# Kernel optimization log

Hardware: AMD Instinct MI355X
Metric: run time of the kernel (lower is better)

## Reference

```python
import jax, jax.numpy as jnp
import numpy as np

Q_SCALE = 64  # 1 << 6, from quantize_8bit default
Q_STEP = 2.0 / Q_SCALE
Q_MIN = -(2 ** 7) / Q_SCALE      # -128/64 = -2.0
Q_MAX = (2 ** 7 - 1) / Q_SCALE   # 127/64


def quantize_8bit(x):
    # round-to-step with straight-through estimator (matches slayer quantize), then clamp
    xq = x + jax.lax.stop_gradient(jnp.round(x / Q_STEP) * Q_STEP - x)
    return jnp.clip(xq, Q_MIN, Q_MAX)


def weight_norm(v, g):
    # per-output-channel weight norm: w = g * v / ||v||  (v: [out, in])
    n = jnp.sqrt(jnp.sum(v * v, axis=1, keepdims=True))
    return g[:, None] * v / n


def sigma_delta_block(x, v, g, clamp6):
    # x: [N, Cin, H, W, T]
    qw = quantize_8bit(weight_norm(v, g))           # [Cout, Cin], 8-bit quantized
    y = jnp.einsum('oi,nihwt->nohwt', qw, x)        # 1x1x1 conv (pointwise)
    s = jnp.cumsum(y, axis=-1)                      # sigma unit: accumulate over time
    mean = jnp.mean(s, axis=(0, 2, 3, 4), keepdims=True)  # mean-only batchnorm
    a = s - mean
    if clamp6:                                      # Clamp6 activation (fc2); Ind = identity (fc1)
        a = jnp.clip(a, -6.0, 6.0)
    # delta unit, threshold=0: d[t] = a[t] - a[t-1], a[-1] = 0
    d = jnp.diff(a, axis=-1, prepend=jnp.zeros_like(a[..., :1]))
    return d


def setup_inputs() -> dict:
    key = jax.random.key(0)
    k = jax.random.split(key, 5)
    N, C, H, W, T = 4, 128, 32, 32, 32
    Cs = 32
    x = jax.random.normal(k[0], (N, C, H, W, T), dtype=jnp.float32)
    v1 = jax.random.normal(k[1], (Cs, C), dtype=jnp.float32) * 0.1
    g1 = jax.random.uniform(k[2], (Cs,), dtype=jnp.float32) + 0.5
    v2 = jax.random.normal(k[3], (C, Cs), dtype=jnp.float32) * 0.1
    g2 = jax.random.uniform(k[4], (C,), dtype=jnp.float32) + 0.5
    return {'x': x, 'v1': v1, 'g1': g1, 'v2': v2, 'g2': g2}


def reference(x, v1, g1, v2, g2):
    h = sigma_delta_block(x, v1, g1, clamp6=False)   # fc1: Ind activation
    out = sigma_delta_block(h, v2, g2, clamp6=True)  # fc2: Clamp6 activation
    return out
```

## Files before the change

kernel.cpp:

```cpp
#include <hip/hip_runtime.h>
#include <hip/hip_cooperative_groups.h>

namespace cg = cooperative_groups;

#define CIN  128
#define CHUNKF 32768

typedef float f32x4 __attribute__((ext_vector_type(4)));
typedef short s16x8 __attribute__((ext_vector_type(8)));


__device__ __forceinline__ uint pack_hilo(float f) {
  uint b = __float_as_uint(f);
  uint hi = b & 0xffff0000u;
  float lo = f - __uint_as_float(hi);
  return (hi >> 16) | (__float_as_uint(lo) & 0xffff0000u);
}

__global__ __launch_bounds__(256) void wnorm_mean_kernel(
    const float* __restrict__ x,
    const float* __restrict__ v1, const float* __restrict__ g1,
    const float* __restrict__ v2, const float* __restrict__ g2,
    float* __restrict__ ws) {
  int tid = threadIdx.x;
  if (blockIdx.x < 2048) {
    int b = blockIdx.x;
    int chunk = b >> 2, quarter = b & 3;
    int i = chunk & 127;
    const float4* xp = (const float4*)(x + (size_t)chunk * CHUNKF + (size_t)quarter * 8192);
    float acc = 0.f;
#pragma unroll
    for (int it = 0; it < 8; ++it) {
      int f4i = tid + 256 * it;
      float4 v = xp[f4i];
      int t0 = (4 * f4i) & 31;
      acc += v.x * (float)(32 - t0) + v.y * (float)(31 - t0)
           + v.z * (float)(30 - t0) + v.w * (float)(29 - t0);
    }
    for (int off = 32; off >= 1; off >>= 1) acc += __shfl_down(acc, off);
    __shared__ float part[4];
    if ((tid & 63) == 0) part[tid >> 6] = acc;
    __syncthreads();
    if (tid == 0) atomicAdd(&ws[8192 + i], part[0] + part[1] + part[2] + part[3]);
  } else {
    int b = blockIdx.x - 2048;
    bool first = (b < 32);
    int row = first ? b : b - 32;
    int len = first ? 128 : 32;
    const float* v = first ? v1 : v2;
    const float* g = first ? g1 : g2;
    double val = 0.0;
    if (tid < len) { double t = (double)v[row * len + tid]; val = t * t; }
    for (int off = 32; off >= 1; off >>= 1) val += __shfl_down(val, off);
    __shared__ double partial[4];
    if ((tid & 63) == 0) partial[tid >> 6] = val;
    __syncthreads();
    double norm = sqrt(partial[0] + partial[1]);
    if (tid < len) {
      double w = (double)g[row] * (double)v[row * len + tid] / norm;
      double qd = rint(w * 32.0) * 0.03125;
      qd = fmin(fmax(qd, -2.0), 1.984375);
      float qf = (float)qd;
      ushort bf = (ushort)(__float_as_uint(qf) >> 16);
      if (first) {
        ws[row * 128 + tid] = qf;
        ((ushort*)(ws + 8448))[row * 128 + tid] = bf;
      } else {
        ws[4096 + row * 32 + tid] = qf;
        ((ushort*)(ws + 10496))[row * 32 + tid] = bf;
      }
    }
  }
}

__global__ __launch_bounds__(256, 4) void fused_kernel(
    const float* __restrict__ x, const float* __restrict__ ws,
    float* __restrict__ out) {
  const ushort* qw1bf = (const ushort*)(ws + 8448);
  const ushort* qw2bf = (const ushort*)(ws + 10496);

  __shared__ uint xs[8192];
  __shared__ float zred[288];
  __shared__ float kls[128];

  const int tid = threadIdx.x;
  const int wv = tid >> 6;
  const int l  = tid & 63;
  const int g  = l >> 4;
  const int ln = l & 15;

  const int nb  = blockIdx.x >> 8;
  const int hw0 = (blockIdx.x & 255) * 4;
  const float* xblk = x + (size_t)nb * CIN * CHUNKF + (size_t)hw0 * 32;

  float4 xr[8];
#pragma unroll
  for (int k = 0; k < 8; ++k) {
    int f = k * 256 + tid, c = f >> 5, n4 = f & 31;
    xr[k] = *(const float4*)(xblk + (size_t)c * CHUNKF + n4 * 4);
  }

  s16x8 A1[2][4];
#pragma unroll
  for (int jt = 0; jt < 2; ++jt)
#pragma unroll
    for (int ks = 0; ks < 4; ++ks)
      A1[jt][ks] = *(const s16x8*)(qw1bf + (jt * 16 + ln) * 128 + ks * 32 + g * 8);

  {
    int j = tid & 31, grp = tid >> 5;
    const float* qr = ws + j * 128 + grp * 16;
    const float* mr = ws + 8192 + grp * 16;
    float pp = 0.f;
#pragma unroll
    for (int cc = 0; cc < 16; ++cc) pp += qr[cc] * mr[cc];
    zred[j * 8 + grp] = pp;
  }
  __syncthreads();
  if (tid < 32) {
    float t = 0.f;
#pragma unroll
    for (int gg = 0; gg < 8; ++gg) t += zred[tid * 8 + gg];
    zred[256 + tid] = t * (1.0f / 131072.0f);
  }
  __syncthreads();
  if (tid < 128) {
    const float* q2 = ws + 4096 + tid * 32;
    float kk = 0.f;
#pragma unroll 8
    for (int j = 0; j < 32; ++j) kk += q2[j] * zred[256 + j];
    kls[tid] = kk;
  }

  f32x4 acc1[2][2];
#pragma unroll
  for (int a = 0; a < 2; ++a)
#pragma unroll
    for (int b = 0; b < 2; ++b) acc1[a][b] = (f32x4){0.f, 0.f, 0.f, 0.f};

#pragma unroll
  for (int ph = 0; ph < 2; ++ph) {
#pragma unroll
    for (int k = 0; k < 8; ++k) {
      int f = k * 256 + tid, c = f >> 5, n4 = f & 31;
      int u = n4 ^ ((c >> 2) & 6);
      uint4 pk;
      pk.x = pack_hilo(xr[k].x); pk.y = pack_hilo(xr[k].y);
      pk.z = pack_hilo(xr[k].z); pk.w = pack_hilo(xr[k].w);
      *(uint4*)&xs[c * 128 + u * 4] = pk;
    }
    __syncthreads();
    if (ph == 0) {
#pragma unroll
      for (int k = 0; k < 8; ++k) {
        int f = k * 256 + tid, c = f >> 5, n4 = f & 31;
        xr[k] = *(const float4*)(xblk + (size_t)(64 + c) * CHUNKF + n4 * 4);
      }
    }
#pragma unroll
    for (int kl = 0; kl < 2; ++kl) {
#pragma unroll
      for (int nt = 0; nt < 2; ++nt) {
        const int n = wv * 32 + nt * 16 + ln;
        const int base = (kl * 32 + g * 8) * 128;
        const int u = ((n >> 2) ^ (((kl * 32 + g * 8) >> 2) & 6)) * 4 + (n & 3);
        uint q0 = xs[base + 0 * 128 + u], q1 = xs[base + 1 * 128 + u];
        uint q2 = xs[base + 2 * 128 + u], q3 = xs[base + 3 * 128 + u];
        uint q4 = xs[base + 4 * 128 + u], q5 = xs[base + 5 * 128 + u];
        uint q6 = xs[base + 6 * 128 + u], q7 = xs[base + 7 * 128 + u];
        uint4 H, L;
        H.x = (q0 & 0xffffu) | (q1 << 16);  H.y = (q2 & 0xffffu) | (q3 << 16);
        H.z = (q4 & 0xffffu) | (q5 << 16);  H.w = (q6 & 0xffffu) | (q7 << 16);
        L.x = (q0 >> 16) | (q1 & 0xffff0000u); L.y = (q2 >> 16) | (q3 & 0xffff0000u);
        L.z = (q4 >> 16) | (q5 & 0xffff0000u); L.w = (q6 >> 16) | (q7 & 0xffff0000u);
        s16x8 Bh = __builtin_bit_cast(s16x8, H);
        s16x8 Bl = __builtin_bit_cast(s16x8, L);
#pragma unroll
        for (int jt = 0; jt < 2; ++jt) {
          acc1[jt][nt] = __builtin_amdgcn_mfma_f32_16x16x32_bf16(A1[jt][ph * 2 + kl], Bh, acc1[jt][nt], 0, 0, 0);
          acc1[jt][nt] = __builtin_amdgcn_mfma_f32_16x16x32_bf16(A1[jt][ph * 2 + kl], Bl, acc1[jt][nt], 0, 0, 0);
        }
      }
    }
    __syncthreads();
  }

  uint* zw = xs + wv * 1024;
#pragma unroll
  for (int jt = 0; jt < 2; ++jt)
#pragma unroll
    for (int nt = 0; nt < 2; ++nt) {
      int n = nt * 16 + ln;
      int u = (jt * 4 + g) ^ (n & 7);
      uint4 pk;
      pk.x = pack_hilo(acc1[jt][nt][0]);
      pk.y = pack_hilo(acc1[jt][nt][1]);
      pk.z = pack_hilo(acc1[jt][nt][2]);
      pk.w = pack_hilo(acc1[jt][nt][3]);
      *(uint4*)&zw[n * 32 + u * 4] = pk;
    }

  s16x8 Ah[2], Al[2];
#pragma unroll
  for (int mt = 0; mt < 2; ++mt) {
    int n = mt * 16 + ln;
    int u0 = (2 * g) ^ (n & 7);
    int u1 = (2 * g + 1) ^ (n & 7);
    uint4 qa = *(const uint4*)&zw[n * 32 + u0 * 4];
    uint4 qb = *(const uint4*)&zw[n * 32 + u1 * 4];
    uint4 H, L;
    H.x = (qa.x & 0xffffu) | (qa.y << 16);  H.y = (qa.z & 0xffffu) | (qa.w << 16);
    H.z = (qb.x & 0xffffu) | (qb.y << 16);  H.w = (qb.z & 0xffffu) | (qb.w << 16);
    L.x = (qa.x >> 16) | (qa.y & 0xffff0000u); L.y = (qa.z >> 16) | (qa.w & 0xffff0000u);
    L.z = (qb.x >> 16) | (qb.y & 0xffff0000u); L.w = (qb.z >> 16) | (qb.w & 0xffff0000u);
    Ah[mt] = __builtin_bit_cast(s16x8, H);
    Al[mt] = __builtin_bit_cast(s16x8, L);
  }

  const size_t outbase = (size_t)nb * CIN * CHUNKF + (size_t)(hw0 + wv) * 32;
#pragma unroll 1
  for (int h = 0; h < 2; ++h) {
    s16x8 B2[4];
#pragma unroll
    for (int q = 0; q < 4; ++q)
      B2[q] = *(const s16x8*)(qw2bf + ((h * 4 + q) * 16 + ln) * 32 + g * 8);
    f32x4 acc2[4][2];
#pragma unroll
    for (int a = 0; a < 4; ++a)
#pragma unroll
      for (int b = 0; b < 2; ++b) acc2[a][b] = (f32x4){0.f, 0.f, 0.f, 0.f};
#pragma unroll
    for (int mt = 0; mt < 2; ++mt)
#pragma unroll
      for (int q = 0; q < 4; ++q) {
        acc2[q][mt] = __builtin_amdgcn_mfma_f32_16x16x32_bf16(Ah[mt], B2[q], acc2[q][mt], 0, 0, 0);
        acc2[q][mt] = __builtin_amdgcn_mfma_f32_16x16x32_bf16(Al[mt], B2[q], acc2[q][mt], 0, 0, 0);
      }
#pragma unroll
    for (int q = 0; q < 4; ++q) {
      const int nt = h * 4 + q;
      float c0[2], c1[2], c2[2], c3[2], base[2], Qi0 = 0.f;
#pragma unroll
      for (int mt = 0; mt < 2; ++mt) {
        c0[mt] = acc2[q][mt][0];
        c1[mt] = c0[mt] + acc2[q][mt][1];
        c2[mt] = c1[mt] + acc2[q][mt][2];
        c3[mt] = c2[mt] + acc2[q][mt][3];
        float Qi = c3[mt];
        float t1 = __shfl_up(Qi, 16); if (g >= 1) Qi += t1;
        float t2 = __shfl_up(Qi, 32); if (g >= 2) Qi += t2;
        base[mt] = Qi - c3[mt];
        if (mt == 0) Qi0 = Qi;
      }
      float S0tot = __shfl(Qi0, 48 + ln);
      base[1] += S0tot;
      const float kpp = kls[nt * 16 + ln];
      float* op = out + outbase + (size_t)(nt * 16 + ln) * CHUNKF;
#pragma unroll
      for (int mt = 0; mt < 2; ++mt) {
        float Bv = base[mt] - kpp;
        float prev = fminf(fmaxf(Bv, -6.f), 6.f);
        if (mt == 0 && g == 0) prev = 0.f;
        float A0 = fminf(fmaxf(Bv + c0[mt], -6.f), 6.f);
        float A1v = fminf(fmaxf(Bv + c1[mt], -6.f), 6.f);
        float A2v = fminf(fmaxf(Bv + c2[mt], -6.f), 6.f);
        float A3v = fminf(fmaxf(Bv + c3[mt], -6.f), 6.f);
        *(float4*)(op + mt * 16 + g * 4) =
            make_float4(A0 - prev, A1v - A0, A2v - A1v, A3v - A2v);
      }
    }
  }
}

__global__ __launch_bounds__(256, 2) void fused_all(
    const float* __restrict__ x,
    const float* __restrict__ v1, const float* __restrict__ g1,
    const float* __restrict__ v2, const float* __restrict__ g2,
    float* __restrict__ ws, float* __restrict__ out) {
  __shared__ uint xs[8192];
  __shared__ float mls[128];
  __shared__ float zred[256];
  __shared__ float zsm[32];
  __shared__ float kls[128];
  __shared__ double wpart[4];

  const int tid = threadIdx.x;
  const int bid = blockIdx.x;
  const int nb  = bid >> 7;
  const int hw8 = (bid & 127) * 8;
  float* msumP = ws + 8192;

  {
    const int l63 = tid & 63, wvp = tid >> 6;
    const int t0 = (4 * l63) & 31;
    const float wt0 = (float)(32 - t0), wt1 = (float)(31 - t0);
    const float wt2 = (float)(30 - t0), wt3 = (float)(29 - t0);
    const int slot = bid & 31;
    const float* xsl = x + (size_t)nb * CIN * CHUNKF + (size_t)hw8 * 32 + l63 * 4;
#pragma unroll 4
    for (int k = 0; k < 32; ++k) {
      int c = k * 4 + wvp;
      float4 v = *(const float4*)(xsl + (size_t)c * CHUNKF);
      float pv = v.x * wt0 + v.y * wt1 + v.z * wt2 + v.w * wt3;
      pv += __shfl_down(pv, 32);
      pv += __shfl_down(pv, 16);
      pv += __shfl_down(pv, 8);
      pv += __shfl_down(pv, 4);
      pv += __shfl_down(pv, 2);
      pv += __shfl_down(pv, 1);
      if (l63 == 0) atomicAdd(&msumP[slot * 128 + c], pv);
    }
  }

  if (bid < 160) {
    bool first = (bid < 32);
    int row = first ? bid : bid - 32;
    int len = first ? 128 : 32;
    const float* v = first ? v1 : v2;
    const float* g = first ? g1 : g2;
    double val = 0.0;
    if (tid < len) { double t = (double)v[row * len + tid]; val = t * t; }
    for (int off = 32; off >= 1; off >>= 1) val += __shfl_down(val, off);
    if ((tid & 63) == 0) wpart[tid >> 6] = val;
    __syncthreads();
    double norm = sqrt(wpart[0] + wpart[1]);
    if (tid < len) {
      double w = (double)g[row] * (double)v[row * len + tid] / norm;
      double qd = rint(w * 32.0) * 0.03125;
      qd = fmin(fmax(qd, -2.0), 1.984375);
      float qf = (float)qd;
      ushort bf = (ushort)(__float_as_uint(qf) >> 16);
      if (first) {
        ws[row * 128 + tid] = qf;
        ((ushort*)(ws + 12544))[row * 128 + tid] = bf;
      } else {
        ws[4096 + row * 32 + tid] = qf;
        ((ushort*)(ws + 14592))[row * 32 + tid] = bf;
      }
    }
  }

  cg::this_grid().sync();

  const ushort* qw1bf = (const ushort*)(ws + 12544);
  const ushort* qw2bf = (const ushort*)(ws + 14592);
  const int wv = tid >> 6;
  const int l  = tid & 63;
  const int g  = l >> 4;
  const int ln = l & 15;

  s16x8 A1[2][4];
#pragma unroll
  for (int jt = 0; jt < 2; ++jt)
#pragma unroll
    for (int ks = 0; ks < 4; ++ks)
      A1[jt][ks] = *(const s16x8*)(qw1bf + (jt * 16 + ln) * 128 + ks * 32 + g * 8);

  float4 xr[8];
  {
    const float* xg = x + (size_t)nb * CIN * CHUNKF + (size_t)hw8 * 32;
#pragma unroll
    for (int k = 0; k < 8; ++k) {
      int f = k * 256 + tid, c = f >> 5, n4 = f & 31;
      xr[k] = *(const float4*)(xg + (size_t)c * CHUNKF + n4 * 4);
    }
  }

  if (tid < 128) {
    float m = 0.f;
#pragma unroll
    for (int p = 0; p < 32; ++p) m += msumP[p * 128 + tid];
    mls[tid] = m;
  }
  __syncthreads();
  {
    int j = tid & 31, grp8 = tid >> 5;
    const float* qr = ws + j * 128 + grp8 * 16;
    float pp = 0.f;
#pragma unroll
    for (int cc = 0; cc < 16; ++cc) pp += qr[cc] * mls[grp8 * 16 + cc];
    zred[j * 8 + grp8] = pp;
  }
  __syncthreads();
  if (tid < 32) {
    float t = 0.f;
#pragma unroll
    for (int gg = 0; gg < 8; ++gg) t += zred[tid * 8 + gg];
    zsm[tid] = t * (1.0f / 131072.0f);
  }
  __syncthreads();
  if (tid < 128) {
    const float* q2p = ws + 4096 + tid * 32;
    float kk = 0.f;
#pragma unroll 8
    for (int j = 0; j < 32; ++j) kk += q2p[j] * zsm[j];
    kls[tid] = kk;
  }

#pragma unroll 1
  for (int grp = 0; grp < 2; ++grp) {
    const int hw0 = hw8 + grp * 4;
    const float* xg = x + (size_t)nb * CIN * CHUNKF + (size_t)hw0 * 32;

    f32x4 acc1[2][2];
#pragma unroll
    for (int a = 0; a < 2; ++a)
#pragma unroll
      for (int b = 0; b < 2; ++b) acc1[a][b] = (f32x4){0.f, 0.f, 0.f, 0.f};

    __syncthreads();

#pragma unroll
    for (int ph = 0; ph < 2; ++ph) {
#pragma unroll
      for (int k = 0; k < 8; ++k) {
        int f = k * 256 + tid, c = f >> 5, n4 = f & 31;
        int u = n4 ^ ((c >> 2) & 6);
        uint4 pk;
        pk.x = pack_hilo(xr[k].x); pk.y = pack_hilo(xr[k].y);
        pk.z = pack_hilo(xr[k].z); pk.w = pack_hilo(xr[k].w);
        *(uint4*)&xs[c * 128 + u * 4] = pk;
      }
      __syncthreads();
      if (ph == 0) {
#pragma unroll
        for (int k = 0; k < 8; ++k) {
          int f = k * 256 + tid, c = f >> 5, n4 = f & 31;
          xr[k] = *(const float4*)(xg + (size_t)(64 + c) * CHUNKF + n4 * 4);
        }
      }
#pragma unroll
      for (int kl = 0; kl < 2; ++kl) {
#pragma unroll
        for (int nt = 0; nt < 2; ++nt) {
          const int n = wv * 32 + nt * 16 + ln;
          const int base = (kl * 32 + g * 8) * 128;
          const int u = ((n >> 2) ^ (((kl * 32 + g * 8) >> 2) & 6)) * 4 + (n & 3);
          uint q0 = xs[base + 0 * 128 + u], q1 = xs[base + 1 * 128 + u];
          uint q2 = xs[base + 2 * 128 + u], q3 = xs[base + 3 * 128 + u];
          uint q4 = xs[base + 4 * 128 + u], q5 = xs[base + 5 * 128 + u];
          uint q6 = xs[base + 6 * 128 + u], q7 = xs[base + 7 * 128 + u];
          uint4 H, L;
          H.x = (q0 & 0xffffu) | (q1 << 16);  H.y = (q2 & 0xffffu) | (q3 << 16);
          H.z = (q4 & 0xffffu) | (q5 << 16);  H.w = (q6 & 0xffffu) | (q7 << 16);
          L.x = (q0 >> 16) | (q1 & 0xffff0000u); L.y = (q2 >> 16) | (q3 & 0xffff0000u);
          L.z = (q4 >> 16) | (q5 & 0xffff0000u); L.w = (q6 >> 16) | (q7 & 0xffff0000u);
          s16x8 Bh = __builtin_bit_cast(s16x8, H);
          s16x8 Bl = __builtin_bit_cast(s16x8, L);
#pragma unroll
          for (int jt = 0; jt < 2; ++jt) {
            acc1[jt][nt] = __builtin_amdgcn_mfma_f32_16x16x32_bf16(A1[jt][ph * 2 + kl], Bh, acc1[jt][nt], 0, 0, 0);
            acc1[jt][nt] = __builtin_amdgcn_mfma_f32_16x16x32_bf16(A1[jt][ph * 2 + kl], Bl, acc1[jt][nt], 0, 0, 0);
          }
        }
      }
      __syncthreads();
    }

    uint* zw = xs + wv * 1024;
#pragma unroll
    for (int jt = 0; jt < 2; ++jt)
#pragma unroll
      for (int nt = 0; nt < 2; ++nt) {
        int n = nt * 16 + ln;
        int u = (jt * 4 + g) ^ (n & 7);
        uint4 pk;
        pk.x = pack_hilo(acc1[jt][nt][0]);
        pk.y = pack_hilo(acc1[jt][nt][1]);
        pk.z = pack_hilo(acc1[jt][nt][2]);
        pk.w = pack_hilo(acc1[jt][nt][3]);
        *(uint4*)&zw[n * 32 + u * 4] = pk;
      }

    s16x8 Ah[2], Al[2];
#pragma unroll
    for (int mt = 0; mt < 2; ++mt) {
      int n = mt * 16 + ln;
      int u0 = (2 * g) ^ (n & 7);
      int u1 = (2 * g + 1) ^ (n & 7);
      uint4 qa = *(const uint4*)&zw[n * 32 + u0 * 4];
      uint4 qb = *(const uint4*)&zw[n * 32 + u1 * 4];
      uint4 H, L;
      H.x = (qa.x & 0xffffu) | (qa.y << 16);  H.y = (qa.z & 0xffffu) | (qa.w << 16);
      H.z = (qb.x & 0xffffu) | (qb.y << 16);  H.w = (qb.z & 0xffffu) | (qb.w << 16);
      L.x = (qa.x >> 16) | (qa.y & 0xffff0000u); L.y = (qa.z >> 16) | (qa.w & 0xffff0000u);
      L.z = (qb.x >> 16) | (qb.y & 0xffff0000u); L.w = (qb.z >> 16) | (qb.w & 0xffff0000u);
      Ah[mt] = __builtin_bit_cast(s16x8, H);
      Al[mt] = __builtin_bit_cast(s16x8, L);
    }

    if (grp == 0) {
      const float* xg1 = x + (size_t)nb * CIN * CHUNKF + (size_t)(hw8 + 4) * 32;
#pragma unroll
      for (int k = 0; k < 8; ++k) {
        int f = k * 256 + tid, c = f >> 5, n4 = f & 31;
        xr[k] = *(const float4*)(xg1 + (size_t)c * CHUNKF + n4 * 4);
      }
    }

    const size_t outbase = (size_t)nb * CIN * CHUNKF + (size_t)(hw0 + wv) * 32;
#pragma unroll 1
    for (int h = 0; h < 2; ++h) {
      s16x8 B2[4];
#pragma unroll
      for (int q = 0; q < 4; ++q)
        B2[q] = *(const s16x8*)(qw2bf + ((h * 4 + q) * 16 + ln) * 32 + g * 8);
      f32x4 acc2[4][2];
#pragma unroll
      for (int a = 0; a < 4; ++a)
#pragma unroll
        for (int b = 0; b < 2; ++b) acc2[a][b] = (f32x4){0.f, 0.f, 0.f, 0.f};
#pragma unroll
      for (int mt = 0; mt < 2; ++mt)
#pragma unroll
        for (int q = 0; q < 4; ++q) {
          acc2[q][mt] = __builtin_amdgcn_mfma_f32_16x16x32_bf16(Ah[mt], B2[q], acc2[q][mt], 0, 0, 0);
          acc2[q][mt] = __builtin_amdgcn_mfma_f32_16x16x32_bf16(Al[mt], B2[q], acc2[q][mt], 0, 0, 0);
        }
#pragma unroll
      for (int q = 0; q < 4; ++q) {
        const int nt = h * 4 + q;
        float c0[2], c1[2], c2[2], c3[2], base[2], Qi0 = 0.f;
#pragma unroll
        for (int mt = 0; mt < 2; ++mt) {
          c0[mt] = acc2[q][mt][0];
          c1[mt] = c0[mt] + acc2[q][mt][1];
          c2[mt] = c1[mt] + acc2[q][mt][2];
          c3[mt] = c2[mt] + acc2[q][mt][3];
          float Qi = c3[mt];
          float t1 = __shfl_up(Qi, 16); if (g >= 1) Qi += t1;
          float t2 = __shfl_up(Qi, 32); if (g >= 2) Qi += t2;
          base[mt] = Qi - c3[mt];
          if (mt == 0) Qi0 = Qi;
        }
        float S0tot = __shfl(Qi0, 48 + ln);
        base[1] += S0tot;
        const float kpp = kls[nt * 16 + ln];
        float* op = out + outbase + (size_t)(nt * 16 + ln) * CHUNKF;
#pragma unroll
        for (int mt = 0; mt < 2; ++mt) {
          float Bv = base[mt] - kpp;
          float prev = fminf(fmaxf(Bv, -6.f), 6.f);
          if (mt == 0 && g == 0) prev = 0.f;
          float A0 = fminf(fmaxf(Bv + c0[mt], -6.f), 6.f);
          float A1v = fminf(fmaxf(Bv + c1[mt], -6.f), 6.f);
          float A2v = fminf(fmaxf(Bv + c2[mt], -6.f), 6.f);
          float A3v = fminf(fmaxf(Bv + c3[mt], -6.f), 6.f);
          *(float4*)(op + mt * 16 + g * 4) =
              make_float4(A0 - prev, A1v - A0, A2v - A1v, A3v - A2v);
        }
      }
    }
  }
}

extern "C" void kernel_launch(void* const* d_in, const int* in_sizes, int n_in,
                              void* d_out, int out_size, void* d_ws, size_t ws_size,
                              hipStream_t stream) {
  const float* x  = (const float*)d_in[0];
  const float* v1 = (const float*)d_in[1];
  const float* g1 = (const float*)d_in[2];
  const float* v2 = (const float*)d_in[3];
  const float* g2 = (const float*)d_in[4];
  float* ws  = (float*)d_ws;
  float* out = (float*)d_out;

  hipMemsetAsync(ws + 8192, 0, 4096 * sizeof(float), stream);

  int dev = 0, coop = 0, occ = 0;
  hipGetDevice(&dev);
  hipDeviceGetAttribute(&coop, hipDeviceAttributeCooperativeLaunch, dev);
  hipOccupancyMaxActiveBlocksPerMultiprocessor(&occ, fused_all, 256, 0);

  if (coop && occ >= 2) {
    void* args[] = { (void*)&x, (void*)&v1, (void*)&g1, (void*)&v2, (void*)&g2,
                     (void*)&ws, (void*)&out };
    hipError_t e = hipLaunchCooperativeKernel((const void*)fused_all, dim3(512),
                                              dim3(256), args, 0, stream);
    if (e == hipSuccess) return;
  }

  wnorm_mean_kernel<<<2208, 256, 0, stream>>>(x, v1, g1, v2, g2, ws);
  fused_kernel<<<1024, 256, 0, stream>>>(x, ws, out);
}
```

Before: 49.28 us.

## Replace cooperative grid sync with atomic-counter spin barrier and split weight-norm kernel

Drops the cooperative launch and grid.sync in favour of a small weight-norm/init kernel plus a 1024-block main kernel. The main kernel increments a global counter after its mean-partial atomics, then spins on that counter before it needs the mean. Stage-1 MFMA work runs before the wait, so the global reduction overlaps with compute. Each block now handles 4 hw positions instead of 8, targeting 4 blocks per CU. The spin barrier relies on all 1024 blocks being co-resident, which is only guarded by an occupancy check, and it has a guard counter that can silently give wrong results on timeout. The fallback path now memsets only 128 floats instead of 4096, which may leave stale partial sums.

```diff
diff --git a/kernel.cpp b/kernel.cpp
--- a/kernel.cpp
+++ b/kernel.cpp
@@ -1,7 +1,4 @@
 #include <hip/hip_runtime.h>
-#include <hip/hip_cooperative_groups.h>
-
-namespace cg = cooperative_groups;
 
 #define CIN  128
 #define CHUNKF 32768
@@ -15,6 +12,283 @@
   uint hi = b & 0xffff0000u;
   float lo = f - __uint_as_float(hi);
   return (hi >> 16) | (__float_as_uint(lo) & 0xffff0000u);
+}
+
+__global__ __launch_bounds__(128) void wnorm_init(
+    const float* __restrict__ v1, const float* __restrict__ g1,
+    const float* __restrict__ v2, const float* __restrict__ g2,
+    float* __restrict__ ws) {
+  int b = blockIdx.x, tid = threadIdx.x;
+  if (b < 32) ws[8192 + b * 128 + tid] = 0.f;
+  if (b == 32 && tid == 0) *(uint*)(ws + 12288) = 0u;
+  bool first = (b < 32);
+  int row = first ? b : b - 32;
+  int len = first ? 128 : 32;
+  const float* v = first ? v1 : v2;
+  const float* g = first ? g1 : g2;
+
+  double val = 0.0;
+  if (tid < len) { double t = (double)v[row * len + tid]; val = t * t; }
+  for (int off = 32; off >= 1; off >>= 1) val += __shfl_down(val, off);
+  __shared__ double partial[2];
+  if ((tid & 63) == 0) partial[tid >> 6] = val;
+  __syncthreads();
+  double norm = sqrt(partial[0] + partial[1]);
+  if (tid < len) {
+    double w = (double)g[row] * (double)v[row * len + tid] / norm;
+    double qd = rint(w * 32.0) * 0.03125;
+    qd = fmin(fmax(qd, -2.0), 1.984375);
+    float qf = (float)qd;
+    ushort bf = (ushort)(__float_as_uint(qf) >> 16);
+    if (first) {
+      ws[row * 128 + tid] = qf;
+      ((ushort*)(ws + 12544))[row * 128 + tid] = bf;
+    } else {
+      ws[4096 + row * 32 + tid] = qf;
+      ((ushort*)(ws + 14592))[row * 32 + tid] = bf;
+    }
+  }
+}
+
+__global__ __launch_bounds__(256, 4) void fused_main(
+    const float* __restrict__ x, float* __restrict__ ws,
+    float* __restrict__ out) {
+  const ushort* qw1bf = (const ushort*)(ws + 12544);
+  const ushort* qw2bf = (const ushort*)(ws + 14592);
+
+  __shared__ uint xs[8192];
+  __shared__ float mls[128];
+  __shared__ float zred[288];
+  __shared__ float kls[128];
+
+  const int tid = threadIdx.x;
+  const int wv = tid >> 6;
+  const int l  = tid & 63;
+  const int g  = l >> 4;
+  const int ln = l & 15;
+
+  const int nb  = blockIdx.x >> 8;
+  const int hw0 = (blockIdx.x & 255) * 4;
+  const float* xblk = x + (size_t)nb * CIN * CHUNKF + (size_t)hw0 * 32;
+  float* msumP = ws + 8192;
+
+  {
+    const int l31 = tid & 31;
+    const int t0 = (l31 & 7) * 4;
+    const float wt0 = (float)(32 - t0), wt1 = (float)(31 - t0);
+    const float wt2 = (float)(30 - t0), wt3 = (float)(29 - t0);
+    const int slot = blockIdx.x & 31;
+#pragma unroll 4
+    for (int k = 0; k < 16; ++k) {
+      int c = k * 8 + (tid >> 5);
+      float4 v = *(const float4*)(xblk + (size_t)c * CHUNKF + l31 * 4);
+      float pv = v.x * wt0 + v.y * wt1 + v.z * wt2 + v.w * wt3;
+      pv += __shfl_down(pv, 16, 32);
+      pv += __shfl_down(pv, 8, 32);
+      pv += __shfl_down(pv, 4, 32);
+      pv += __shfl_down(pv, 2, 32);
+      pv += __shfl_down(pv, 1, 32);
+      if (l31 == 0) atomicAdd(&msumP[slot * 128 + c], pv);
+    }
+  }
+  __threadfence();
+  __syncthreads();
+  if (tid == 0) atomicAdd((uint*)(ws + 12288), 1u);
+
+  float4 xr[8];
+#pragma unroll
+  for (int k = 0; k < 8; ++k) {
+    int f = k * 256 + tid, c = f >> 5, n4 = f & 31;
+    xr[k] = *(const float4*)(xblk + (size_t)c * CHUNKF + n4 * 4);
+  }
+
+  s16x8 A1[2][4];
+#pragma unroll
+  for (int jt = 0; jt < 2; ++jt)
+#pragma unroll
+    for (int ks = 0; ks < 4; ++ks)
+      A1[jt][ks] = *(const s16x8*)(qw1bf + (jt * 16 + ln) * 128 + ks * 32 + g * 8);
+
+  f32x4 acc1[2][2];
+#pragma unroll
+  for (int a = 0; a < 2; ++a)
+#pragma unroll
+    for (int b = 0; b < 2; ++b) acc1[a][b] = (f32x4){0.f, 0.f, 0.f, 0.f};
+
+#pragma unroll
+  for (int ph = 0; ph < 2; ++ph) {
+#pragma unroll
+    for (int k = 0; k < 8; ++k) {
+      int f = k * 256 + tid, c = f >> 5, n4 = f & 31;
+      int u = n4 ^ ((c >> 2) & 6);
+      uint4 pk;
+      pk.x = pack_hilo(xr[k].x); pk.y = pack_hilo(xr[k].y);
+      pk.z = pack_hilo(xr[k].z); pk.w = pack_hilo(xr[k].w);
+      *(uint4*)&xs[c * 128 + u * 4] = pk;
+    }
+    __syncthreads();
+    if (ph == 0) {
+#pragma unroll
+      for (int k = 0; k < 8; ++k) {
+        int f = k * 256 + tid, c = f >> 5, n4 = f & 31;
+        xr[k] = *(const float4*)(xblk + (size_t)(64 + c) * CHUNKF + n4 * 4);
+      }
+    }
+#pragma unroll
+    for (int kl = 0; kl < 2; ++kl) {
+#pragma unroll
+      for (int nt = 0; nt < 2; ++nt) {
+        const int n = wv * 32 + nt * 16 + ln;
+        const int base = (kl * 32 + g * 8) * 128;
+        const int u = ((n >> 2) ^ (((kl * 32 + g * 8) >> 2) & 6)) * 4 + (n & 3);
+        uint q0 = xs[base + 0 * 128 + u], q1 = xs[base + 1 * 128 + u];
+        uint q2 = xs[base + 2 * 128 + u], q3 = xs[base + 3 * 128 + u];
+        uint q4 = xs[base + 4 * 128 + u], q5 = xs[base + 5 * 128 + u];
+        uint q6 = xs[base + 6 * 128 + u], q7 = xs[base + 7 * 128 + u];
+        uint4 H, L;
+        H.x = (q0 & 0xffffu) | (q1 << 16);  H.y = (q2 & 0xffffu) | (q3 << 16);
+        H.z = (q4 & 0xffffu) | (q5 << 16);  H.w = (q6 & 0xffffu) | (q7 << 16);
+        L.x = (q0 >> 16) | (q1 & 0xffff0000u); L.y = (q2 >> 16) | (q3 & 0xffff0000u);
+        L.z = (q4 >> 16) | (q5 & 0xffff0000u); L.w = (q6 >> 16) | (q7 & 0xffff0000u);
+        s16x8 Bh = __builtin_bit_cast(s16x8, H);
+        s16x8 Bl = __builtin_bit_cast(s16x8, L);
+#pragma unroll
+        for (int jt = 0; jt < 2; ++jt) {
+          acc1[jt][nt] = __builtin_amdgcn_mfma_f32_16x16x32_bf16(A1[jt][ph * 2 + kl], Bh, acc1[jt][nt], 0, 0, 0);
+          acc1[jt][nt] = __builtin_amdgcn_mfma_f32_16x16x32_bf16(A1[jt][ph * 2 + kl], Bl, acc1[jt][nt], 0, 0, 0);
+        }
+      }
+    }
+    __syncthreads();
+  }
+
+  uint* zw = xs + wv * 1024;
+#pragma unroll
+  for (int jt = 0; jt < 2; ++jt)
+#pragma unroll
+    for (int nt = 0; nt < 2; ++nt) {
+      int n = nt * 16 + ln;
+      int u = (jt * 4 + g) ^ (n & 7);
+      uint4 pk;
+      pk.x = pack_hilo(acc1[jt][nt][0]);
+      pk.y = pack_hilo(acc1[jt][nt][1]);
+      pk.z = pack_hilo(acc1[jt][nt][2]);
+      pk.w = pack_hilo(acc1[jt][nt][3]);
+      *(uint4*)&zw[n * 32 + u * 4] = pk;
+    }
+
+  s16x8 Ah[2], Al[2];
+#pragma unroll
+  for (int mt = 0; mt < 2; ++mt) {
+    int n = mt * 16 + ln;
+    int u0 = (2 * g) ^ (n & 7);
+    int u1 = (2 * g + 1) ^ (n & 7);
+    uint4 qa = *(const uint4*)&zw[n * 32 + u0 * 4];
+    uint4 qb = *(const uint4*)&zw[n * 32 + u1 * 4];
+    uint4 H, L;
+    H.x = (qa.x & 0xffffu) | (qa.y << 16);  H.y = (qa.z & 0xffffu) | (qa.w << 16);
+    H.z = (qb.x & 0xffffu) | (qb.y << 16);  H.w = (qb.z & 0xffffu) | (qb.w << 16);
+    L.x = (qa.x >> 16) | (qa.y & 0xffff0000u); L.y = (qa.z >> 16) | (qa.w & 0xffff0000u);
+    L.z = (qb.x >> 16) | (qb.y & 0xffff0000u); L.w = (qb.z >> 16) | (qb.w & 0xffff0000u);
+    Ah[mt] = __builtin_bit_cast(s16x8, H);
+    Al[mt] = __builtin_bit_cast(s16x8, L);
+  }
+
+  if (tid == 0) {
+    const uint* dc = (const uint*)(ws + 12288);
+    int guard = 0;
+    while (__hip_atomic_load(dc, __ATOMIC_ACQUIRE, __HIP_MEMORY_SCOPE_AGENT) < 1024u
+           && ++guard < 10000000) { }
+  }
+  __syncthreads();
+  __threadfence();
+  if (tid < 128) {
+    float m = 0.f;
+#pragma unroll
+    for (int p = 0; p < 32; ++p)
+      m += __hip_atomic_load(&msumP[p * 128 + tid], __ATOMIC_RELAXED,
+                             __HIP_MEMORY_SCOPE_AGENT);
+    mls[tid] = m * (1.0f / 131072.0f);
+  }
+  __syncthreads();
+  {
+    int j = tid & 31, grp = tid >> 5;
+    const float* qr = ws + j * 128 + grp * 16;
+    float pp = 0.f;
+#pragma unroll
+    for (int cc = 0; cc < 16; ++cc) pp += qr[cc] * mls[grp * 16 + cc];
+    zred[j * 8 + grp] = pp;
+  }
+  __syncthreads();
+  if (tid < 32) {
+    float t = 0.f;
+#pragma unroll
+    for (int gg = 0; gg < 8; ++gg) t += zred[tid * 8 + gg];
+    zred[256 + tid] = t;
+  }
+  __syncthreads();
+  if (tid < 128) {
+    const float* q2 = ws + 4096 + tid * 32;
+    float kk = 0.f;
+#pragma unroll 8
+    for (int j = 0; j < 32; ++j) kk += q2[j] * zred[256 + j];
+    kls[tid] = kk;
+  }
+  __syncthreads();
+
+  const size_t outbase = (size_t)nb * CIN * CHUNKF + (size_t)(hw0 + wv) * 32;
+#pragma unroll 1
+  for (int h = 0; h < 2; ++h) {
+    s16x8 B2[4];
+#pragma unroll
+    for (int q = 0; q < 4; ++q)
+      B2[q] = *(const s16x8*)(qw2bf + ((h * 4 + q) * 16 + ln) * 32 + g * 8);
+    f32x4 acc2[4][2];
+#pragma unroll
+    for (int a = 0; a < 4; ++a)
+#pragma unroll
+      for (int b = 0; b < 2; ++b) acc2[a][b] = (f32x4){0.f, 0.f, 0.f, 0.f};
+#pragma unroll
+    for (int mt = 0; mt < 2; ++mt)
+#pragma unroll
+      for (int q = 0; q < 4; ++q) {
+        acc2[q][mt] = __builtin_amdgcn_mfma_f32_16x16x32_bf16(Ah[mt], B2[q], acc2[q][mt], 0, 0, 0);
+        acc2[q][mt] = __builtin_amdgcn_mfma_f32_16x16x32_bf16(Al[mt], B2[q], acc2[q][mt], 0, 0, 0);
+      }
+#pragma unroll
+    for (int q = 0; q < 4; ++q) {
+      const int nt = h * 4 + q;
+      float c0[2], c1[2], c2[2], c3[2], base[2], Qi0 = 0.f;
+#pragma unroll
+      for (int mt = 0; mt < 2; ++mt) {
+        c0[mt] = acc2[q][mt][0];
+        c1[mt] = c0[mt] + acc2[q][mt][1];
+        c2[mt] = c1[mt] + acc2[q][mt][2];
+        c3[mt] = c2[mt] + acc2[q][mt][3];
+        float Qi = c3[mt];
+        float t1 = __shfl_up(Qi, 16); if (g >= 1) Qi += t1;
+        float t2 = __shfl_up(Qi, 32); if (g >= 2) Qi += t2;
+        base[mt] = Qi - c3[mt];
+        if (mt == 0) Qi0 = Qi;
+      }
+      float S0tot = __shfl(Qi0, 48 + ln);
+      base[1] += S0tot;
+      const float kpp = kls[nt * 16 + ln];
+      float* op = out + outbase + (size_t)(nt * 16 + ln) * CHUNKF;
+#pragma unroll
+      for (int mt = 0; mt < 2; ++mt) {
+        float Bv = base[mt] - kpp;
+        float prev = fminf(fmaxf(Bv, -6.f), 6.f);
+        if (mt == 0 && g == 0) prev = 0.f;
+        float A0 = fminf(fmaxf(Bv + c0[mt], -6.f), 6.f);
+        float A1v = fminf(fmaxf(Bv + c1[mt], -6.f), 6.f);
+        float A2v = fminf(fmaxf(Bv + c2[mt], -6.f), 6.f);
+        float A3v = fminf(fmaxf(Bv + c3[mt], -6.f), 6.f);
+        *(float4*)(op + mt * 16 + g * 4) =
+            make_float4(A0 - prev, A1v - A0, A2v - A1v, A3v - A2v);
+      }
+    }
+  }
 }
 
 __global__ __launch_bounds__(256) void wnorm_mean_kernel(
@@ -272,288 +546,6 @@
   }
 }
 
-__global__ __launch_bounds__(256, 2) void fused_all(
-    const float* __restrict__ x,
-    const float* __restrict__ v1, const float* __restrict__ g1,
-    const float* __restrict__ v2, const float* __restrict__ g2,
-    float* __restrict__ ws, float* __restrict__ out) {
-  __shared__ uint xs[8192];
-  __shared__ float mls[128];
-  __shared__ float zred[256];
-  __shared__ float zsm[32];
-  __shared__ float kls[128];
-  __shared__ double wpart[4];
-
-  const int tid = threadIdx.x;
-  const int bid = blockIdx.x;
-  const int nb  = bid >> 7;
-  const int hw8 = (bid & 127) * 8;
-  float* msumP = ws + 8192;
-
-  {
-    const int l63 = tid & 63, wvp = tid >> 6;
-    const int t0 = (4 * l63) & 31;
-    const float wt0 = (float)(32 - t0), wt1 = (float)(31 - t0);
-    const float wt2 = (float)(30 - t0), wt3 = (float)(29 - t0);
-    const int slot = bid & 31;
-    const float* xsl = x + (size_t)nb * CIN * CHUNKF + (size_t)hw8 * 32 + l63 * 4;
-#pragma unroll 4
-    for (int k = 0; k < 32; ++k) {
-      int c = k * 4 + wvp;
-      float4 v = *(const float4*)(xsl + (size_t)c * CHUNKF);
-      float pv = v.x * wt0 + v.y * wt1 + v.z * wt2 + v.w * wt3;
-      pv += __shfl_down(pv, 32);
-      pv += __shfl_down(pv, 16);
-      pv += __shfl_down(pv, 8);
-      pv += __shfl_down(pv, 4);
-      pv += __shfl_down(pv, 2);
-      pv += __shfl_down(pv, 1);
-      if (l63 == 0) atomicAdd(&msumP[slot * 128 + c], pv);
-    }
-  }
-
-  if (bid < 160) {
-    bool first = (bid < 32);
-    int row = first ? bid : bid - 32;
-    int len = first ? 128 : 32;
-    const float* v = first ? v1 : v2;
-    const float* g = first ? g1 : g2;
-    double val = 0.0;
-    if (tid < len) { double t = (double)v[row * len + tid]; val = t * t; }
-    for (int off = 32; off >= 1; off >>= 1) val += __shfl_down(val, off);
-    if ((tid & 63) == 0) wpart[tid >> 6] = val;
-    __syncthreads();
-    double norm = sqrt(wpart[0] + wpart[1]);
-    if (tid < len) {
-      double w = (double)g[row] * (double)v[row * len + tid] / norm;
-      double qd = rint(w * 32.0) * 0.03125;
-      qd = fmin(fmax(qd, -2.0), 1.984375);
-      float qf = (float)qd;
-      ushort bf = (ushort)(__float_as_uint(qf) >> 16);
-      if (first) {
-        ws[row * 128 + tid] = qf;
-        ((ushort*)(ws + 12544))[row * 128 + tid] = bf;
-      } else {
-        ws[4096 + row * 32 + tid] = qf;
-        ((ushort*)(ws + 14592))[row * 32 + tid] = bf;
-      }
-    }
-  }
-
-  cg::this_grid().sync();
-
-  const ushort* qw1bf = (const ushort*)(ws + 12544);
-  const ushort* qw2bf = (const ushort*)(ws + 14592);
-  const int wv = tid >> 6;
-  const int l  = tid & 63;
-  const int g  = l >> 4;
-  const int ln = l & 15;
-
-  s16x8 A1[2][4];
-#pragma unroll
-  for (int jt = 0; jt < 2; ++jt)
-#pragma unroll
-    for (int ks = 0; ks < 4; ++ks)
-      A1[jt][ks] = *(const s16x8*)(qw1bf + (jt * 16 + ln) * 128 + ks * 32 + g * 8);
-
-  float4 xr[8];
-  {
-    const float* xg = x + (size_t)nb * CIN * CHUNKF + (size_t)hw8 * 32;
-#pragma unroll
-    for (int k = 0; k < 8; ++k) {
-      int f = k * 256 + tid, c = f >> 5, n4 = f & 31;
-      xr[k] = *(const float4*)(xg + (size_t)c * CHUNKF + n4 * 4);
-    }
-  }
-
-  if (tid < 128) {
-    float m = 0.f;
-#pragma unroll
-    for (int p = 0; p < 32; ++p) m += msumP[p * 128 + tid];
-    mls[tid] = m;
-  }
-  __syncthreads();
-  {
-    int j = tid & 31, grp8 = tid >> 5;
-    const float* qr = ws + j * 128 + grp8 * 16;
-    float pp = 0.f;
-#pragma unroll
-    for (int cc = 0; cc < 16; ++cc) pp += qr[cc] * mls[grp8 * 16 + cc];
-    zred[j * 8 + grp8] = pp;
-  }
-  __syncthreads();
-  if (tid < 32) {
-    float t = 0.f;
-#pragma unroll
-    for (int gg = 0; gg < 8; ++gg) t += zred[tid * 8 + gg];
-    zsm[tid] = t * (1.0f / 131072.0f);
-  }
-  __syncthreads();
-  if (tid < 128) {
-    const float* q2p = ws + 4096 + tid * 32;
-    float kk = 0.f;
-#pragma unroll 8
-    for (int j = 0; j < 32; ++j) kk += q2p[j] * zsm[j];
-    kls[tid] = kk;
-  }
-
-#pragma unroll 1
-  for (int grp = 0; grp < 2; ++grp) {
-    const int hw0 = hw8 + grp * 4;
-    const float* xg = x + (size_t)nb * CIN * CHUNKF + (size_t)hw0 * 32;
-
-    f32x4 acc1[2][2];
-#pragma unroll
-    for (int a = 0; a < 2; ++a)
-#pragma unroll
-      for (int b = 0; b < 2; ++b) acc1[a][b] = (f32x4){0.f, 0.f, 0.f, 0.f};
-
-    __syncthreads();
-
-#pragma unroll
-    for (int ph = 0; ph < 2; ++ph) {
-#pragma unroll
-      for (int k = 0; k < 8; ++k) {
-        int f = k * 256 + tid, c = f >> 5, n4 = f & 31;
-        int u = n4 ^ ((c >> 2) & 6);
-        uint4 pk;
-        pk.x = pack_hilo(xr[k].x); pk.y = pack_hilo(xr[k].y);
-        pk.z = pack_hilo(xr[k].z); pk.w = pack_hilo(xr[k].w);
-        *(uint4*)&xs[c * 128 + u * 4] = pk;
-      }
-      __syncthreads();
-      if (ph == 0) {
-#pragma unroll
-        for (int k = 0; k < 8; ++k) {
-          int f = k * 256 + tid, c = f >> 5, n4 = f & 31;
-          xr[k] = *(const float4*)(xg + (size_t)(64 + c) * CHUNKF + n4 * 4);
-        }
-      }
-#pragma unroll
-      for (int kl = 0; kl < 2; ++kl) {
-#pragma unroll
-        for (int nt = 0; nt < 2; ++nt) {
-          const int n = wv * 32 + nt * 16 + ln;
-          const int base = (kl * 32 + g * 8) * 128;
-          const int u = ((n >> 2) ^ (((kl * 32 + g * 8) >> 2) & 6)) * 4 + (n & 3);
-          uint q0 = xs[base + 0 * 128 + u], q1 = xs[base + 1 * 128 + u];
-          uint q2 = xs[base + 2 * 128 + u], q3 = xs[base + 3 * 128 + u];
-          uint q4 = xs[base + 4 * 128 + u], q5 = xs[base + 5 * 128 + u];
-          uint q6 = xs[base + 6 * 128 + u], q7 = xs[base + 7 * 128 + u];
-          uint4 H, L;
-          H.x = (q0 & 0xffffu) | (q1 << 16);  H.y = (q2 & 0xffffu) | (q3 << 16);
-          H.z = (q4 & 0xffffu) | (q5 << 16);  H.w = (q6 & 0xffffu) | (q7 << 16);
-          L.x = (q0 >> 16) | (q1 & 0xffff0000u); L.y = (q2 >> 16) | (q3 & 0xffff0000u);
-          L.z = (q4 >> 16) | (q5 & 0xffff0000u); L.w = (q6 >> 16) | (q7 & 0xffff0000u);
-          s16x8 Bh = __builtin_bit_cast(s16x8, H);
-          s16x8 Bl = __builtin_bit_cast(s16x8, L);
-#pragma unroll
-          for (int jt = 0; jt < 2; ++jt) {
-            acc1[jt][nt] = __builtin_amdgcn_mfma_f32_16x16x32_bf16(A1[jt][ph * 2 + kl], Bh, acc1[jt][nt], 0, 0, 0);
-            acc1[jt][nt] = __builtin_amdgcn_mfma_f32_16x16x32_bf16(A1[jt][ph * 2 + kl], Bl, acc1[jt][nt], 0, 0, 0);
-          }
-        }
-      }
-      __syncthreads();
-    }
-
-    uint* zw = xs + wv * 1024;
-#pragma unroll
-    for (int jt = 0; jt < 2; ++jt)
-#pragma unroll
-      for (int nt = 0; nt < 2; ++nt) {
-        int n = nt * 16 + ln;
-        int u = (jt * 4 + g) ^ (n & 7);
-        uint4 pk;
-        pk.x = pack_hilo(acc1[jt][nt][0]);
-        pk.y = pack_hilo(acc1[jt][nt][1]);
-        pk.z = pack_hilo(acc1[jt][nt][2]);
-        pk.w = pack_hilo(acc1[jt][nt][3]);
-        *(uint4*)&zw[n * 32 + u * 4] = pk;
-      }
-
-    s16x8 Ah[2], Al[2];
-#pragma unroll
-    for (int mt = 0; mt < 2; ++mt) {
-      int n = mt * 16 + ln;
-      int u0 = (2 * g) ^ (n & 7);
-      int u1 = (2 * g + 1) ^ (n & 7);
-      uint4 qa = *(const uint4*)&zw[n * 32 + u0 * 4];
-      uint4 qb = *(const uint4*)&zw[n * 32 + u1 * 4];
-      uint4 H, L;
-      H.x = (qa.x & 0xffffu) | (qa.y << 16);  H.y = (qa.z & 0xffffu) | (qa.w << 16);
-      H.z = (qb.x & 0xffffu) | (qb.y << 16);  H.w = (qb.z & 0xffffu) | (qb.w << 16);
-      L.x = (qa.x >> 16) | (qa.y & 0xffff0000u); L.y = (qa.z >> 16) | (qa.w & 0xffff0000u);
-      L.z = (qb.x >> 16) | (qb.y & 0xffff0000u); L.w = (qb.z >> 16) | (qb.w & 0xffff0000u);
-      Ah[mt] = __builtin_bit_cast(s16x8, H);
-      Al[mt] = __builtin_bit_cast(s16x8, L);
-    }
-
-    if (grp == 0) {
-      const float* xg1 = x + (size_t)nb * CIN * CHUNKF + (size_t)(hw8 + 4) * 32;
-#pragma unroll
-      for (int k = 0; k < 8; ++k) {
-        int f = k * 256 + tid, c = f >> 5, n4 = f & 31;
-        xr[k] = *(const float4*)(xg1 + (size_t)c * CHUNKF + n4 * 4);
-      }
-    }
-
-    const size_t outbase = (size_t)nb * CIN * CHUNKF + (size_t)(hw0 + wv) * 32;
-#pragma unroll 1
-    for (int h = 0; h < 2; ++h) {
-      s16x8 B2[4];
-#pragma unroll
-      for (int q = 0; q < 4; ++q)
-        B2[q] = *(const s16x8*)(qw2bf + ((h * 4 + q) * 16 + ln) * 32 + g * 8);
-      f32x4 acc2[4][2];
-#pragma unroll
-      for (int a = 0; a < 4; ++a)
-#pragma unroll
-        for (int b = 0; b < 2; ++b) acc2[a][b] = (f32x4){0.f, 0.f, 0.f, 0.f};
-#pragma unroll
-      for (int mt = 0; mt < 2; ++mt)
-#pragma unroll
-        for (int q = 0; q < 4; ++q) {
-          acc2[q][mt] = __builtin_amdgcn_mfma_f32_16x16x32_bf16(Ah[mt], B2[q], acc2[q][mt], 0, 0, 0);
-          acc2[q][mt] = __builtin_amdgcn_mfma_f32_16x16x32_bf16(Al[mt], B2[q], acc2[q][mt], 0, 0, 0);
-        }
-#pragma unroll
-      for (int q = 0; q < 4; ++q) {
-        const int nt = h * 4 + q;
-        float c0[2], c1[2], c2[2], c3[2], base[2], Qi0 = 0.f;
-#pragma unroll
-        for (int mt = 0; mt < 2; ++mt) {
-          c0[mt] = acc2[q][mt][0];
-          c1[mt] = c0[mt] + acc2[q][mt][1];
-          c2[mt] = c1[mt] + acc2[q][mt][2];
-          c3[mt] = c2[mt] + acc2[q][mt][3];
-          float Qi = c3[mt];
-          float t1 = __shfl_up(Qi, 16); if (g >= 1) Qi += t1;
-          float t2 = __shfl_up(Qi, 32); if (g >= 2) Qi += t2;
-          base[mt] = Qi - c3[mt];
-          if (mt == 0) Qi0 = Qi;
-        }
-        float S0tot = __shfl(Qi0, 48 + ln);
-        base[1] += S0tot;
-        const float kpp = kls[nt * 16 + ln];
-        float* op = out + outbase + (size_t)(nt * 16 + ln) * CHUNKF;
-#pragma unroll
-        for (int mt = 0; mt < 2; ++mt) {
-          float Bv = base[mt] - kpp;
-          float prev = fminf(fmaxf(Bv, -6.f), 6.f);
-          if (mt == 0 && g == 0) prev = 0.f;
-          float A0 = fminf(fmaxf(Bv + c0[mt], -6.f), 6.f);
-          float A1v = fminf(fmaxf(Bv + c1[mt], -6.f), 6.f);
-          float A2v = fminf(fmaxf(Bv + c2[mt], -6.f), 6.f);
-          float A3v = fminf(fmaxf(Bv + c3[mt], -6.f), 6.f);
-          *(float4*)(op + mt * 16 + g * 4) =
-              make_float4(A0 - prev, A1v - A0, A2v - A1v, A3v - A2v);
-        }
-      }
-    }
-  }
-}
-
 extern "C" void kernel_launch(void* const* d_in, const int* in_sizes, int n_in,
                               void* d_out, int out_size, void* d_ws, size_t ws_size,
                               hipStream_t stream) {
@@ -565,21 +557,15 @@
   float* ws  = (float*)d_ws;
   float* out = (float*)d_out;
 
-  hipMemsetAsync(ws + 8192, 0, 4096 * sizeof(float), stream);
-
-  int dev = 0, coop = 0, occ = 0;
-  hipGetDevice(&dev);
-  hipDeviceGetAttribute(&coop, hipDeviceAttributeCooperativeLaunch, dev);
-  hipOccupancyMaxActiveBlocksPerMultiprocessor(&occ, fused_all, 256, 0);
-
-  if (coop && occ >= 2) {
-    void* args[] = { (void*)&x, (void*)&v1, (void*)&g1, (void*)&v2, (void*)&g2,
-                     (void*)&ws, (void*)&out };
-    hipError_t e = hipLaunchCooperativeKernel((const void*)fused_all, dim3(512),
-                                              dim3(256), args, 0, stream);
-    if (e == hipSuccess) return;
-  }
-
-  wnorm_mean_kernel<<<2208, 256, 0, stream>>>(x, v1, g1, v2, g2, ws);
-  fused_kernel<<<1024, 256, 0, stream>>>(x, ws, out);
+  int occ = 0;
+  hipOccupancyMaxActiveBlocksPerMultiprocessor(&occ, fused_main, 256, 0);
+
+  if (occ >= 4) {
+    wnorm_init<<<160, 128, 0, stream>>>(v1, g1, v2, g2, ws);
+    fused_main<<<1024, 256, 0, stream>>>(x, ws, out);
+  } else {
+    hipMemsetAsync(ws + 8192, 0, 128 * sizeof(float), stream);
+    wnorm_mean_kernel<<<2208, 256, 0, stream>>>(x, v1, g1, v2, g2, ws);
+    fused_kernel<<<1024, 256, 0, stream>>>(x, ws, out);
+  }
 }
```

Result: no change. 48.76 us (-1.0%).
